# Optimization experiments

Hardware: AMD Instinct MI355X
Metric: run time of the kernel (lower is better)

Reference implementation:

```python
import jax, jax.numpy as jnp
import numpy as np

N_NODES = 100000
N_EDGES = 1600000
D = 64            # embedding_dim
D2 = D * D        # GRUCell hidden/input size


def gru_cell(x, h, w_ih, w_hh, b_ih, b_hh):
    # PyTorch GRUCell math. x, h: [D2]; w_ih, w_hh: [3*D2, D2]; b_*: [3*D2]
    gi = w_ih @ x + b_ih
    gh = w_hh @ h + b_hh
    i_r, i_z, i_n = jnp.split(gi, 3)
    h_r, h_z, h_n = jnp.split(gh, 3)
    r = jax.nn.sigmoid(i_r + h_r)
    z = jax.nn.sigmoid(i_z + h_z)
    n = jnp.tanh(i_n + r * h_n)
    return (1.0 - z) * n + z * h


def gcn_layer(x, w, src, dst, edge_norm):
    # dense transform then degree-normalized gather-scatter aggregation
    h = x @ w                                   # [N, D]
    m = h[src] * edge_norm[:, None]             # [E, D] messages
    return jax.ops.segment_sum(m, dst, num_segments=N_NODES)


def setup_inputs() -> dict:
    key = jax.random.key(0)
    ks = jax.random.split(key, 12)
    s = 0.02  # keep GRU gates in a sane range
    return {
        "node_embeddings": jax.random.normal(ks[0], (N_NODES, D), jnp.float32),
        "gc1_weights": jax.random.normal(ks[1], (D, D), jnp.float32) * s,
        "gc2_weights": jax.random.normal(ks[2], (D, D), jnp.float32) * s,
        "gc1_hist": jax.random.normal(ks[3], (D, D), jnp.float32) * s,
        "gc2_hist": jax.random.normal(ks[4], (D, D), jnp.float32) * s,
        "w_ih": jax.random.normal(ks[5], (3 * D2, D2), jnp.float32) * s,
        "w_hh": jax.random.normal(ks[6], (3 * D2, D2), jnp.float32) * s,
        "b_ih": jax.random.normal(ks[7], (3 * D2,), jnp.float32) * s,
        "b_hh": jax.random.normal(ks[8], (3 * D2,), jnp.float32) * s,
        "src": jax.random.randint(ks[9], (N_EDGES,), 0, N_NODES, jnp.int32),
        "dst": jax.random.randint(ks[10], (N_EDGES,), 0, N_NODES, jnp.int32),
    }


def reference(node_embeddings, gc1_weights, gc2_weights, gc1_hist, gc2_hist,
              w_ih, w_hh, b_ih, b_hh, src, dst):
    # --- weight evolution (GRUCell over flattened GCN weights) ---
    w1 = gru_cell(gc1_hist.reshape(-1), gc1_weights.reshape(-1),
                  w_ih, w_hh, b_ih, b_hh).reshape(D, D)
    w2 = gru_cell(gc2_hist.reshape(-1), gc2_weights.reshape(-1),
                  w_ih, w_hh, b_ih, b_hh).reshape(D, D)

    # --- symmetric degree normalization (in-degree, clamped at 1) ---
    deg = jax.ops.segment_sum(jnp.ones_like(dst, jnp.float32), dst,
                              num_segments=N_NODES)
    norm = jnp.clip(deg, 1.0, None) ** -0.5     # [N]
    edge_norm = norm[src] * norm[dst]           # [E]

    # --- two GCN layers ---
    x = jax.nn.relu(gcn_layer(node_embeddings, w1, src, dst, edge_norm))
    x = gcn_layer(x, w2, src, dst, edge_norm)
    return x
```

## Files before the change

### kernel.cpp

```cpp
#include <hip/hip_runtime.h>

typedef unsigned int uint_t;
typedef float v4f __attribute__((ext_vector_type(4)));

#define N_NODES 100000
#define N_EDGES 1600000
#define D 64
#define D2 4096
#define D3 12288

#define NPAD 100352u

#define BSHIFT 9
#define BNODES 512
#define NBUCK 196
#define CHUNK 8192
#define CAP   16384
#define GRUBLK 3072

#define OFF_GI1   0u
#define OFF_GI2   (OFF_GI1 + D3)
#define OFF_GH1   (OFF_GI2 + D3)
#define OFF_GH2   (OFF_GH1 + D3)
#define OFF_DEG   (OFF_GH2 + D3)
#define OFF_BCUR  (OFF_DEG + NPAD)
#define OFF_ROWS  (OFF_BCUR + 256u)
#define OFF_CSR   (OFF_ROWS + NPAD)
#define OFF_H     (OFF_CSR + 1600000u)
#define OFF_AGG1  (OFF_H + 3200000u)
#define OFF_PAIRS (OFF_AGG1 + 3200000u)

__device__ __forceinline__ float dot4v(v4f a, float4 b, float acc) {
    acc = fmaf(a[0], b.x, acc);
    acc = fmaf(a[1], b.y, acc);
    acc = fmaf(a[2], b.z, acc);
    acc = fmaf(a[3], b.w, acc);
    return acc;
}

__device__ __forceinline__ uint_t bfr(float f) {
    uint_t u = __float_as_uint(f);
    u += 0x7FFFu + ((u >> 16) & 1u);
    return u >> 16;
}

struct PartLds {
    int hist[256];
    int lbase[256];
    int gbase[256];
    int lcur[256];
    int2 stage[CHUNK];
};
struct GruLds {
    float4 sA[1024];
    float4 sB[1024];
};

__global__ __launch_bounds__(512) void mega1(
    const float* __restrict__ w_ih, const float* __restrict__ w_hh,
    const float* __restrict__ x1, const float* __restrict__ x2,
    const float* __restrict__ h1, const float* __restrict__ h2,
    float* __restrict__ gi1, float* __restrict__ gi2,
    float* __restrict__ gh1, float* __restrict__ gh2,
    const int* __restrict__ src, const int* __restrict__ dst,
    int* __restrict__ deg, int* __restrict__ bcur, int2* __restrict__ pairs)
{
    __shared__ __align__(16) char ldsraw[sizeof(PartLds)];
    const int tid = threadIdx.x;

    if (blockIdx.x < NBUCK) {
        PartLds& P = *reinterpret_cast<PartLds*>(ldsraw);
        const int e0  = blockIdx.x * CHUNK;
        const int cnt = min(CHUNK, N_EDGES - e0);

        if (tid < 256) { P.hist[tid] = 0; P.lcur[tid] = 0; }
        __syncthreads();
        for (int i = tid; i < cnt; i += 512) {
            const int d = dst[e0 + i];
            atomicAdd(&deg[d], 1);
            atomicAdd(&P.hist[d >> BSHIFT], 1);
        }
        __syncthreads();
        if (tid < 256) P.lbase[tid] = P.hist[tid];
        __syncthreads();
        for (int off = 1; off < 256; off <<= 1) {
            int a = 0, b = 0;
            if (tid < 256) { a = P.lbase[tid]; b = (tid >= off) ? P.lbase[tid - off] : 0; }
            __syncthreads();
            if (tid < 256) P.lbase[tid] = a + b;
            __syncthreads();
        }
        if (tid < 256) {
            const int c = P.hist[tid];
            P.lbase[tid] -= c;
            P.gbase[tid] = c ? atomicAdd(&bcur[tid], c) : 0;
        }
        __syncthreads();
        for (int i = tid; i < cnt; i += 512) {
            const int s = src[e0 + i], d = dst[e0 + i];
            const int b = d >> BSHIFT;
            const int p = P.lbase[b] + atomicAdd(&P.lcur[b], 1);
            P.stage[p] = make_int2(s, d);
        }
        __syncthreads();
        for (int i = tid; i < cnt; i += 512) {
            const int2 v = P.stage[i];
            const int b = v.y >> BSHIFT;
            const int gp = P.gbase[b] + (i - P.lbase[b]);
            if (gp < CAP) pairs[(size_t)b * CAP + gp] = v;
        }
    } else {
        GruLds& G = *reinterpret_cast<GruLds*>(ldsraw);
        const int gb   = blockIdx.x - NBUCK;
        const int half = (gb >= GRUBLK / 2);
        const int blk  = gb - (half ? GRUBLK / 2 : 0);

        {
            const float4* va = (const float4*)(half ? h1 : x1);
            const float4* vb = (const float4*)(half ? h2 : x2);
#pragma unroll
            for (int i = 0; i < 2; ++i) {
                const int k = tid + i * 512;
                G.sA[k] = va[k];
                G.sB[k] = vb[k];
            }
        }
        __syncthreads();

        const int wave = tid >> 6, lane = tid & 63;
        const int row  = blk * 8 + wave;
        const v4f* wr = (const v4f*)((half ? w_hh : w_ih) + (size_t)row * D2);

        float p0 = 0.f, p1 = 0.f;
#pragma unroll
        for (int g = 0; g < 4; ++g) {
            v4f a[4];
#pragma unroll
            for (int k = 0; k < 4; ++k)
                a[k] = __builtin_nontemporal_load(&wr[lane + (g * 4 + k) * 64]);
#pragma unroll
            for (int k = 0; k < 4; ++k) {
                const int idx = lane + (g * 4 + k) * 64;
                p0 = dot4v(a[k], G.sA[idx], p0);
                p1 = dot4v(a[k], G.sB[idx], p1);
            }
        }
#pragma unroll
        for (int m = 32; m > 0; m >>= 1) {
            p0 += __shfl_down(p0, m, 64);
            p1 += __shfl_down(p1, m, 64);
        }
        if (lane == 0) {
            float* oA = half ? gh1 : gi1;
            float* oB = half ? gh2 : gi2;
            oA[row] = p0;
            oB[row] = p1;
        }
    }
}

__global__ __launch_bounds__(256) void bucket_csr_kernel(
    const int2* __restrict__ pairs, const int* __restrict__ deg,
    const int* __restrict__ bcnt,
    int* __restrict__ rowstart, int* __restrict__ csr_src)
{
    __shared__ int lofs[BNODES];
    __shared__ int lcur[BNODES];
    __shared__ int pscan[256];
    __shared__ int bscan[256];
    __shared__ int stage[CAP];
    const int tid = threadIdx.x;
    const int b   = blockIdx.x;
    const int nodeBase = b << BSHIFT;

    const int cb = (tid < NBUCK) ? bcnt[tid] : 0;
    bscan[tid] = cb;
    __syncthreads();
    for (int off = 1; off < 256; off <<= 1) {
        int a = bscan[tid];
        int x = (tid >= off) ? bscan[tid - off] : 0;
        __syncthreads();
        bscan[tid] = a + x;
        __syncthreads();
    }
    const int cnt  = bcnt[b];
    const int base = bscan[b] - cnt;

    const int n0 = nodeBase + 2 * tid;
    const int d0 = (n0     < N_NODES) ? deg[n0]     : 0;
    const int d1 = (n0 + 1 < N_NODES) ? deg[n0 + 1] : 0;
    pscan[tid] = d0 + d1;
    __syncthreads();
    for (int off = 1; off < 256; off <<= 1) {
        int a = pscan[tid];
        int x = (tid >= off) ? pscan[tid - off] : 0;
        __syncthreads();
        pscan[tid] = a + x;
        __syncthreads();
    }
    const int ex = pscan[tid] - (d0 + d1);
    lofs[2 * tid]     = ex;
    lofs[2 * tid + 1] = ex + d0;
    lcur[2 * tid]     = 0;
    lcur[2 * tid + 1] = 0;

    if (n0     < N_NODES) rowstart[n0]     = base + ex;
    if (n0 + 1 < N_NODES) rowstart[n0 + 1] = base + ex + d0;
    __syncthreads();

    const int2* bp = pairs + (size_t)b * CAP;
    for (int i = tid; i < cnt; i += 256) {
        const int2 v = bp[i];
        const int ln = v.y - nodeBase;
        const int p  = lofs[ln] + atomicAdd(&lcur[ln], 1);
        stage[p] = v.x;
    }
    __syncthreads();
    for (int i = tid; i < cnt; i += 256)
        csr_src[base + i] = stage[i];
}

template <bool BF16IN>
__global__ __launch_bounds__(256) void transform_kernel(
    const void* __restrict__ xin,
    const float* __restrict__ gi, const float* __restrict__ gh,
    const float* __restrict__ b_ih, const float* __restrict__ b_hh,
    const float* __restrict__ hw,
    const int* __restrict__ deg, unsigned short* __restrict__ outbf)
{
    __shared__ float sw[D * D];
    const int tid = threadIdx.x;
#pragma unroll
    for (int i = 0; i < 16; ++i) {
        const int j = tid + i * 256;
        float ir = gi[j]          + b_ih[j];
        float hr = gh[j]          + b_hh[j];
        float iz = gi[j + D2]     + b_ih[j + D2];
        float hz = gh[j + D2]     + b_hh[j + D2];
        float in_ = gi[j + 2*D2]  + b_ih[j + 2*D2];
        float hn = gh[j + 2*D2]   + b_hh[j + 2*D2];
        float r = 1.f / (1.f + expf(-(ir + hr)));
        float z = 1.f / (1.f + expf(-(iz + hz)));
        float n = tanhf(in_ + r * hn);
        sw[j] = (1.f - z) * n + z * hw[j];
    }
    __syncthreads();

    const int node = blockIdx.x * 256 + tid;
    if (node >= N_NODES) return;

    float x[D];
    if (BF16IN) {
        const uint4* p = (const uint4*)((const unsigned short*)xin + (size_t)node * D);
#pragma unroll
        for (int i = 0; i < 8; ++i) {
            uint4 u = p[i];
            x[i*8+0] = __uint_as_float(u.x << 16);
            x[i*8+1] = __uint_as_float(u.x & 0xFFFF0000u);
            x[i*8+2] = __uint_as_float(u.y << 16);
            x[i*8+3] = __uint_as_float(u.y & 0xFFFF0000u);
            x[i*8+4] = __uint_as_float(u.z << 16);
            x[i*8+5] = __uint_as_float(u.z & 0xFFFF0000u);
            x[i*8+6] = __uint_as_float(u.w << 16);
            x[i*8+7] = __uint_as_float(u.w & 0xFFFF0000u);
        }
    } else {
        const float4* p = (const float4*)((const float*)xin + (size_t)node * D);
#pragma unroll
        for (int i = 0; i < 16; ++i) {
            float4 u = p[i];
            x[i*4+0] = u.x; x[i*4+1] = u.y;
            x[i*4+2] = u.z; x[i*4+3] = u.w;
        }
    }

    float acc[D];
#pragma unroll
    for (int j = 0; j < D; ++j) acc[j] = 0.f;
#pragma unroll
    for (int k = 0; k < D; ++k) {
        float a = x[k];
#pragma unroll
        for (int j = 0; j < D; ++j) acc[j] = fmaf(a, sw[k * D + j], acc[j]);
    }

    const float nn = rsqrtf(fmaxf((float)deg[node], 1.0f));
    uint_t pk[32];
#pragma unroll
    for (int j = 0; j < 32; ++j)
        pk[j] = bfr(acc[2 * j] * nn) | (bfr(acc[2 * j + 1] * nn) << 16);

    uint4* po = (uint4*)(outbf + (size_t)node * D);
#pragma unroll
    for (int i = 0; i < 8; ++i)
        po[i] = make_uint4(pk[4 * i], pk[4 * i + 1], pk[4 * i + 2], pk[4 * i + 3]);
}

template <bool BF16RELU_OUT>
__global__ __launch_bounds__(256) void aggregate_gather(
    const unsigned short* __restrict__ hbf, const int* __restrict__ csr_src,
    const int* __restrict__ rowstart, const int* __restrict__ degv,
    void* __restrict__ out)
{
    const int tid  = threadIdx.x;
    const int node = blockIdx.x * 16 + (tid >> 4);
    if (node >= N_NODES) return;
    const int lg = tid & 15;
    const uint2* hp = (const uint2*)hbf;

    const int beg = rowstart[node];
    const int dg  = degv[node];

    float4 acc = make_float4(0.f, 0.f, 0.f, 0.f);
    int k = 0;
    for (; k + 8 <= dg; k += 8) {
        int s[8];
#pragma unroll
        for (int u = 0; u < 8; ++u) s[u] = csr_src[beg + k + u];
        uint2 r[8];
#pragma unroll
        for (int u = 0; u < 8; ++u) r[u] = hp[(size_t)s[u] * 16 + lg];
#pragma unroll
        for (int u = 0; u < 8; ++u) {
            acc.x += __uint_as_float(r[u].x << 16);
            acc.y += __uint_as_float(r[u].x & 0xFFFF0000u);
            acc.z += __uint_as_float(r[u].y << 16);
            acc.w += __uint_as_float(r[u].y & 0xFFFF0000u);
        }
    }
    for (; k < dg; ++k) {
        const int s = csr_src[beg + k];
        const uint2 r = hp[(size_t)s * 16 + lg];
        acc.x += __uint_as_float(r.x << 16);
        acc.y += __uint_as_float(r.x & 0xFFFF0000u);
        acc.z += __uint_as_float(r.y << 16);
        acc.w += __uint_as_float(r.y & 0xFFFF0000u);
    }

    const float nn = rsqrtf(fmaxf((float)dg, 1.0f));
    if (BF16RELU_OUT) {
        const float ox = fmaxf(acc.x * nn, 0.f);
        const float oy = fmaxf(acc.y * nn, 0.f);
        const float oz = fmaxf(acc.z * nn, 0.f);
        const float ow = fmaxf(acc.w * nn, 0.f);
        uint2 pk;
        pk.x = bfr(ox) | (bfr(oy) << 16);
        pk.y = bfr(oz) | (bfr(ow) << 16);
        ((uint2*)out)[(size_t)node * 16 + lg] = pk;
    } else {
        float4 o = make_float4(acc.x * nn, acc.y * nn, acc.z * nn, acc.w * nn);
        *(float4*)((float*)out + (size_t)node * D + (size_t)lg * 4) = o;
    }
}

extern "C" void kernel_launch(void* const* d_in, const int* in_sizes, int n_in,
                              void* d_out, int out_size, void* d_ws, size_t ws_size,
                              hipStream_t stream)
{
    const float* emb  = (const float*)d_in[0];
    const float* gc1w = (const float*)d_in[1];
    const float* gc2w = (const float*)d_in[2];
    const float* gc1h = (const float*)d_in[3];
    const float* gc2h = (const float*)d_in[4];
    const float* w_ih = (const float*)d_in[5];
    const float* w_hh = (const float*)d_in[6];
    const float* b_ih = (const float*)d_in[7];
    const float* b_hh = (const float*)d_in[8];
    const int* src = (const int*)d_in[9];
    const int* dst = (const int*)d_in[10];

    float* ws = (float*)d_ws;
    float* gi1 = ws + OFF_GI1;
    float* gi2 = ws + OFF_GI2;
    float* gh1 = ws + OFF_GH1;
    float* gh2 = ws + OFF_GH2;
    int*   deg = (int*)(ws + OFF_DEG);
    int*   bcur = (int*)(ws + OFF_BCUR);
    int*   rows = (int*)(ws + OFF_ROWS);
    int*   csr  = (int*)(ws + OFF_CSR);
    unsigned short* hbf  = (unsigned short*)(ws + OFF_H);
    unsigned short* agg1 = (unsigned short*)(ws + OFF_AGG1);
    int2*  pairs = (int2*)(ws + OFF_PAIRS);
    float* out  = (float*)d_out;

    hipMemsetAsync(deg, 0, (NPAD + 256) * sizeof(int), stream);

    mega1<<<NBUCK + GRUBLK, 512, 0, stream>>>(
        w_ih, w_hh, gc1h, gc2h, gc1w, gc2w, gi1, gi2, gh1, gh2,
        src, dst, deg, bcur, pairs);

    bucket_csr_kernel<<<NBUCK, 256, 0, stream>>>(pairs, deg, bcur, rows, csr);

    transform_kernel<false><<<(N_NODES + 255) / 256, 256, 0, stream>>>(
        emb, gi1, gh1, b_ih, b_hh, gc1w, deg, hbf);
    aggregate_gather<true><<<(N_NODES + 15) / 16, 256, 0, stream>>>(
        hbf, csr, rows, deg, agg1);

    transform_kernel<true><<<(N_NODES + 255) / 256, 256, 0, stream>>>(
        agg1, gi2, gh2, b_ih, b_hh, gc2w, deg, hbf);
    aggregate_gather<false><<<(N_NODES + 15) / 16, 256, 0, stream>>>(
        hbf, csr, rows, deg, out);
}
```

Measured before the change: 625.2 us.

## Fuse CSR bucketing with first transform and widen gather loads to 16 bytes

Merges the bucket CSR build and the layer-1 dense transform into one launch. The two block types are independent, so one launch saves a kernel boundary and lets them run side by side, with LDS shared through a raw buffer. The gather kernel now gives each node 8 lanes, each doing uint4 (16-byte) loads, instead of 16 lanes doing uint2 loads. This means fewer lanes and wider memory transactions per edge. The fused kernel's LDS footprint (about 70KB) now also applies to the transform blocks, which may cut their occupancy.

Measured after the change: 619.9 us. No clear change (-0.8%).

```diff
diff --git a/kernel.cpp b/kernel.cpp
--- a/kernel.cpp
+++ b/kernel.cpp
@@ -17,6 +17,7 @@
 #define CHUNK 8192
 #define CAP   16384
 #define GRUBLK 3072
+#define XBLK  ((N_NODES + 255) / 256)
 
 #define OFF_GI1   0u
 #define OFF_GI2   (OFF_GI1 + D3)
@@ -159,70 +160,131 @@
     }
 }
 
-__global__ __launch_bounds__(256) void bucket_csr_kernel(
+struct CsrLds {
+    int lofs[BNODES];
+    int lcur[BNODES];
+    int pscan[256];
+    int bscan[256];
+    int stage[CAP];
+};
+
+__global__ __launch_bounds__(256) void mega2(
     const int2* __restrict__ pairs, const int* __restrict__ deg,
-    const int* __restrict__ bcnt,
-    int* __restrict__ rowstart, int* __restrict__ csr_src)
+    const int* __restrict__ bcnt, int* __restrict__ rowstart,
+    int* __restrict__ csr_src,
+    const float* __restrict__ emb,
+    const float* __restrict__ gi, const float* __restrict__ gh,
+    const float* __restrict__ b_ih, const float* __restrict__ b_hh,
+    const float* __restrict__ hw, unsigned short* __restrict__ outbf)
 {
-    __shared__ int lofs[BNODES];
-    __shared__ int lcur[BNODES];
-    __shared__ int pscan[256];
-    __shared__ int bscan[256];
-    __shared__ int stage[CAP];
+    __shared__ __align__(16) char ldsraw[sizeof(CsrLds)];
     const int tid = threadIdx.x;
-    const int b   = blockIdx.x;
-    const int nodeBase = b << BSHIFT;
-
-    const int cb = (tid < NBUCK) ? bcnt[tid] : 0;
-    bscan[tid] = cb;
-    __syncthreads();
-    for (int off = 1; off < 256; off <<= 1) {
-        int a = bscan[tid];
-        int x = (tid >= off) ? bscan[tid - off] : 0;
-        __syncthreads();
-        bscan[tid] = a + x;
-        __syncthreads();
-    }
-    const int cnt  = bcnt[b];
-    const int base = bscan[b] - cnt;
-
-    const int n0 = nodeBase + 2 * tid;
-    const int d0 = (n0     < N_NODES) ? deg[n0]     : 0;
-    const int d1 = (n0 + 1 < N_NODES) ? deg[n0 + 1] : 0;
-    pscan[tid] = d0 + d1;
-    __syncthreads();
-    for (int off = 1; off < 256; off <<= 1) {
-        int a = pscan[tid];
-        int x = (tid >= off) ? pscan[tid - off] : 0;
-        __syncthreads();
-        pscan[tid] = a + x;
-        __syncthreads();
-    }
-    const int ex = pscan[tid] - (d0 + d1);
-    lofs[2 * tid]     = ex;
-    lofs[2 * tid + 1] = ex + d0;
-    lcur[2 * tid]     = 0;
-    lcur[2 * tid + 1] = 0;
-
-    if (n0     < N_NODES) rowstart[n0]     = base + ex;
-    if (n0 + 1 < N_NODES) rowstart[n0 + 1] = base + ex + d0;
-    __syncthreads();
-
-    const int2* bp = pairs + (size_t)b * CAP;
-    for (int i = tid; i < cnt; i += 256) {
-        const int2 v = bp[i];
-        const int ln = v.y - nodeBase;
-        const int p  = lofs[ln] + atomicAdd(&lcur[ln], 1);
-        stage[p] = v.x;
-    }
-    __syncthreads();
-    for (int i = tid; i < cnt; i += 256)
-        csr_src[base + i] = stage[i];
-}
-
-template <bool BF16IN>
-__global__ __launch_bounds__(256) void transform_kernel(
-    const void* __restrict__ xin,
+
+    if (blockIdx.x < NBUCK) {
+        CsrLds& L = *reinterpret_cast<CsrLds*>(ldsraw);
+        const int b = blockIdx.x;
+        const int nodeBase = b << BSHIFT;
+
+        const int cb = (tid < NBUCK) ? bcnt[tid] : 0;
+        L.bscan[tid] = cb;
+        __syncthreads();
+        for (int off = 1; off < 256; off <<= 1) {
+            int a = L.bscan[tid];
+            int x = (tid >= off) ? L.bscan[tid - off] : 0;
+            __syncthreads();
+            L.bscan[tid] = a + x;
+            __syncthreads();
+        }
+        const int cnt  = bcnt[b];
+        const int base = L.bscan[b] - cnt;
+
+        const int n0 = nodeBase + 2 * tid;
+        const int d0 = (n0     < N_NODES) ? deg[n0]     : 0;
+        const int d1 = (n0 + 1 < N_NODES) ? deg[n0 + 1] : 0;
+        L.pscan[tid] = d0 + d1;
+        __syncthreads();
+        for (int off = 1; off < 256; off <<= 1) {
+            int a = L.pscan[tid];
+            int x = (tid >= off) ? L.pscan[tid - off] : 0;
+            __syncthreads();
+            L.pscan[tid] = a + x;
+            __syncthreads();
+        }
+        const int ex = L.pscan[tid] - (d0 + d1);
+        L.lofs[2 * tid]     = ex;
+        L.lofs[2 * tid + 1] = ex + d0;
+        L.lcur[2 * tid]     = 0;
+        L.lcur[2 * tid + 1] = 0;
+
+        if (n0     < N_NODES) rowstart[n0]     = base + ex;
+        if (n0 + 1 < N_NODES) rowstart[n0 + 1] = base + ex + d0;
+        __syncthreads();
+
+        const int2* bp = pairs + (size_t)b * CAP;
+        for (int i = tid; i < cnt; i += 256) {
+            const int2 v = bp[i];
+            const int ln = v.y - nodeBase;
+            const int p  = L.lofs[ln] + atomicAdd(&L.lcur[ln], 1);
+            L.stage[p] = v.x;
+        }
+        __syncthreads();
+        for (int i = tid; i < cnt; i += 256)
+            csr_src[base + i] = L.stage[i];
+    } else {
+        float* sw = reinterpret_cast<float*>(ldsraw);
+#pragma unroll
+        for (int i = 0; i < 16; ++i) {
+            const int j = tid + i * 256;
+            float ir = gi[j]          + b_ih[j];
+            float hr = gh[j]          + b_hh[j];
+            float iz = gi[j + D2]     + b_ih[j + D2];
+            float hz = gh[j + D2]     + b_hh[j + D2];
+            float in_ = gi[j + 2*D2]  + b_ih[j + 2*D2];
+            float hn = gh[j + 2*D2]   + b_hh[j + 2*D2];
+            float r = 1.f / (1.f + expf(-(ir + hr)));
+            float z = 1.f / (1.f + expf(-(iz + hz)));
+            float n = tanhf(in_ + r * hn);
+            sw[j] = (1.f - z) * n + z * hw[j];
+        }
+        __syncthreads();
+
+        const int node = (blockIdx.x - NBUCK) * 256 + tid;
+        if (node >= N_NODES) return;
+
+        float x[D];
+        const float4* p = (const float4*)(emb + (size_t)node * D);
+#pragma unroll
+        for (int i = 0; i < 16; ++i) {
+            float4 u = p[i];
+            x[i*4+0] = u.x; x[i*4+1] = u.y;
+            x[i*4+2] = u.z; x[i*4+3] = u.w;
+        }
+
+        float acc[D];
+#pragma unroll
+        for (int j = 0; j < D; ++j) acc[j] = 0.f;
+#pragma unroll
+        for (int k = 0; k < D; ++k) {
+            float a = x[k];
+#pragma unroll
+            for (int j = 0; j < D; ++j) acc[j] = fmaf(a, sw[k * D + j], acc[j]);
+        }
+
+        const float nn = rsqrtf(fmaxf((float)deg[node], 1.0f));
+        uint_t pk[32];
+#pragma unroll
+        for (int j = 0; j < 32; ++j)
+            pk[j] = bfr(acc[2 * j] * nn) | (bfr(acc[2 * j + 1] * nn) << 16);
+
+        uint4* po = (uint4*)(outbf + (size_t)node * D);
+#pragma unroll
+        for (int i = 0; i < 8; ++i)
+            po[i] = make_uint4(pk[4*i], pk[4*i+1], pk[4*i+2], pk[4*i+3]);
+    }
+}
+
+__global__ __launch_bounds__(256) void transform2_kernel(
+    const unsigned short* __restrict__ xin,
     const float* __restrict__ gi, const float* __restrict__ gh,
     const float* __restrict__ b_ih, const float* __restrict__ b_hh,
     const float* __restrict__ hw,
@@ -250,28 +312,18 @@
     if (node >= N_NODES) return;
 
     float x[D];
-    if (BF16IN) {
-        const uint4* p = (const uint4*)((const unsigned short*)xin + (size_t)node * D);
-#pragma unroll
-        for (int i = 0; i < 8; ++i) {
-            uint4 u = p[i];
-            x[i*8+0] = __uint_as_float(u.x << 16);
-            x[i*8+1] = __uint_as_float(u.x & 0xFFFF0000u);
-            x[i*8+2] = __uint_as_float(u.y << 16);
-            x[i*8+3] = __uint_as_float(u.y & 0xFFFF0000u);
-            x[i*8+4] = __uint_as_float(u.z << 16);
-            x[i*8+5] = __uint_as_float(u.z & 0xFFFF0000u);
-            x[i*8+6] = __uint_as_float(u.w << 16);
-            x[i*8+7] = __uint_as_float(u.w & 0xFFFF0000u);
-        }
-    } else {
-        const float4* p = (const float4*)((const float*)xin + (size_t)node * D);
-#pragma unroll
-        for (int i = 0; i < 16; ++i) {
-            float4 u = p[i];
-            x[i*4+0] = u.x; x[i*4+1] = u.y;
-            x[i*4+2] = u.z; x[i*4+3] = u.w;
-        }
+    const uint4* p = (const uint4*)(xin + (size_t)node * D);
+#pragma unroll
+    for (int i = 0; i < 8; ++i) {
+        uint4 u = p[i];
+        x[i*8+0] = __uint_as_float(u.x << 16);
+        x[i*8+1] = __uint_as_float(u.x & 0xFFFF0000u);
+        x[i*8+2] = __uint_as_float(u.y << 16);
+        x[i*8+3] = __uint_as_float(u.y & 0xFFFF0000u);
+        x[i*8+4] = __uint_as_float(u.z << 16);
+        x[i*8+5] = __uint_as_float(u.z & 0xFFFF0000u);
+        x[i*8+6] = __uint_as_float(u.w << 16);
+        x[i*8+7] = __uint_as_float(u.w & 0xFFFF0000u);
     }
 
     float acc[D];
@@ -293,7 +345,7 @@
     uint4* po = (uint4*)(outbf + (size_t)node * D);
 #pragma unroll
     for (int i = 0; i < 8; ++i)
-        po[i] = make_uint4(pk[4 * i], pk[4 * i + 1], pk[4 * i + 2], pk[4 * i + 3]);
+        po[i] = make_uint4(pk[4*i], pk[4*i+1], pk[4*i+2], pk[4*i+3]);
 }
 
 template <bool BF16RELU_OUT>
@@ -303,53 +355,66 @@
     void* __restrict__ out)
 {
     const int tid  = threadIdx.x;
-    const int node = blockIdx.x * 16 + (tid >> 4);
+    const int node = blockIdx.x * 32 + (tid >> 3);
     if (node >= N_NODES) return;
-    const int lg = tid & 15;
-    const uint2* hp = (const uint2*)hbf;
+    const int lg = tid & 7;
+    const uint4* hp = (const uint4*)hbf;
 
     const int beg = rowstart[node];
     const int dg  = degv[node];
 
-    float4 acc = make_float4(0.f, 0.f, 0.f, 0.f);
+    float acc[8];
+#pragma unroll
+    for (int c = 0; c < 8; ++c) acc[c] = 0.f;
+
     int k = 0;
     for (; k + 8 <= dg; k += 8) {
         int s[8];
 #pragma unroll
         for (int u = 0; u < 8; ++u) s[u] = csr_src[beg + k + u];
-        uint2 r[8];
-#pragma unroll
-        for (int u = 0; u < 8; ++u) r[u] = hp[(size_t)s[u] * 16 + lg];
+        uint4 r[8];
+#pragma unroll
+        for (int u = 0; u < 8; ++u) r[u] = hp[(size_t)s[u] * 8 + lg];
 #pragma unroll
         for (int u = 0; u < 8; ++u) {
-            acc.x += __uint_as_float(r[u].x << 16);
-            acc.y += __uint_as_float(r[u].x & 0xFFFF0000u);
-            acc.z += __uint_as_float(r[u].y << 16);
-            acc.w += __uint_as_float(r[u].y & 0xFFFF0000u);
+            acc[0] += __uint_as_float(r[u].x << 16);
+            acc[1] += __uint_as_float(r[u].x & 0xFFFF0000u);
+            acc[2] += __uint_as_float(r[u].y << 16);
+            acc[3] += __uint_as_float(r[u].y & 0xFFFF0000u);
+            acc[4] += __uint_as_float(r[u].z << 16);
+            acc[5] += __uint_as_float(r[u].z & 0xFFFF0000u);
+            acc[6] += __uint_as_float(r[u].w << 16);
+            acc[7] += __uint_as_float(r[u].w & 0xFFFF0000u);
         }
     }
     for (; k < dg; ++k) {
         const int s = csr_src[beg + k];
-        const uint2 r = hp[(size_t)s * 16 + lg];
-        acc.x += __uint_as_float(r.x << 16);
-        acc.y += __uint_as_float(r.x & 0xFFFF0000u);
-        acc.z += __uint_as_float(r.y << 16);
-        acc.w += __uint_as_float(r.y & 0xFFFF0000u);
+        const uint4 r = hp[(size_t)s * 8 + lg];
+        acc[0] += __uint_as_float(r.x << 16);
+        acc[1] += __uint_as_float(r.x & 0xFFFF0000u);
+        acc[2] += __uint_as_float(r.y << 16);
+        acc[3] += __uint_as_float(r.y & 0xFFFF0000u);
+        acc[4] += __uint_as_float(r.z << 16);
+        acc[5] += __uint_as_float(r.z & 0xFFFF0000u);
+        acc[6] += __uint_as_float(r.w << 16);
+        acc[7] += __uint_as_float(r.w & 0xFFFF0000u);
     }
 
     const float nn = rsqrtf(fmaxf((float)dg, 1.0f));
     if (BF16RELU_OUT) {
-        const float ox = fmaxf(acc.x * nn, 0.f);
-        const float oy = fmaxf(acc.y * nn, 0.f);
-        const float oz = fmaxf(acc.z * nn, 0.f);
-        const float ow = fmaxf(acc.w * nn, 0.f);
-        uint2 pk;
-        pk.x = bfr(ox) | (bfr(oy) << 16);
-        pk.y = bfr(oz) | (bfr(ow) << 16);
-        ((uint2*)out)[(size_t)node * 16 + lg] = pk;
+        float o[8];
+#pragma unroll
+        for (int c = 0; c < 8; ++c) o[c] = fmaxf(acc[c] * nn, 0.f);
+        uint4 pk;
+        pk.x = bfr(o[0]) | (bfr(o[1]) << 16);
+        pk.y = bfr(o[2]) | (bfr(o[3]) << 16);
+        pk.z = bfr(o[4]) | (bfr(o[5]) << 16);
+        pk.w = bfr(o[6]) | (bfr(o[7]) << 16);
+        ((uint4*)out)[(size_t)node * 8 + lg] = pk;
     } else {
-        float4 o = make_float4(acc.x * nn, acc.y * nn, acc.z * nn, acc.w * nn);
-        *(float4*)((float*)out + (size_t)node * D + (size_t)lg * 4) = o;
+        float* op = (float*)out + (size_t)node * D + (size_t)lg * 8;
+        *(float4*)(op)     = make_float4(acc[0]*nn, acc[1]*nn, acc[2]*nn, acc[3]*nn);
+        *(float4*)(op + 4) = make_float4(acc[4]*nn, acc[5]*nn, acc[6]*nn, acc[7]*nn);
     }
 }
 
@@ -389,15 +454,15 @@
         w_ih, w_hh, gc1h, gc2h, gc1w, gc2w, gi1, gi2, gh1, gh2,
         src, dst, deg, bcur, pairs);
 
-    bucket_csr_kernel<<<NBUCK, 256, 0, stream>>>(pairs, deg, bcur, rows, csr);
-
-    transform_kernel<false><<<(N_NODES + 255) / 256, 256, 0, stream>>>(
-        emb, gi1, gh1, b_ih, b_hh, gc1w, deg, hbf);
-    aggregate_gather<true><<<(N_NODES + 15) / 16, 256, 0, stream>>>(
+    mega2<<<NBUCK + XBLK, 256, 0, stream>>>(
+        pairs, deg, bcur, rows, csr,
+        emb, gi1, gh1, b_ih, b_hh, gc1w, hbf);
+
+    aggregate_gather<true><<<(N_NODES + 31) / 32, 256, 0, stream>>>(
         hbf, csr, rows, deg, agg1);
 
-    transform_kernel<true><<<(N_NODES + 255) / 256, 256, 0, stream>>>(
+    transform2_kernel<<<XBLK, 256, 0, stream>>>(
         agg1, gi2, gh2, b_ih, b_hh, gc2w, deg, hbf);
-    aggregate_gather<false><<<(N_NODES + 15) / 16, 256, 0, stream>>>(
+    aggregate_gather<false><<<(N_NODES + 31) / 32, 256, 0, stream>>>(
         hbf, csr, rows, deg, out);
 }
```
